# Kernel optimization log

Measured on AMD Instinct MI355X. Metric: run time of the kernel, lower is better.

## Reference

```python
import jax, jax.numpy as jnp
from jax import lax
import numpy as np

T, B, I, H = 512, 64, 512, 512


def setup_inputs() -> dict:
    key = jax.random.key(0)
    k0, k1, k2, k3, k4 = jax.random.split(key, 5)
    s = 1.0 / np.sqrt(H)  # PyTorch LSTM init range
    x = jax.random.normal(k0, (T, B, I), dtype=jnp.float32)
    W_ih = jax.random.uniform(k1, (4 * H, I), jnp.float32, -s, s)
    W_hh = jax.random.uniform(k2, (4 * H, H), jnp.float32, -s, s)
    b_ih = jax.random.uniform(k3, (4 * H,), jnp.float32, -s, s)
    b_hh = jax.random.uniform(k4, (4 * H,), jnp.float32, -s, s)
    return {"x": x, "W_ih": W_ih, "W_hh": W_hh, "b_ih": b_ih, "b_hh": b_hh}


def reference(x, W_ih, W_hh, b_ih, b_hh):
    # x: [T, B, I] (seq-first, like nn.LSTM with batch_first=False)
    Bv = x.shape[1]
    Hv = W_hh.shape[1]
    # Precompute input projections for all timesteps: [T, B, 4H]
    x_proj = jnp.einsum('tbi,gi->tbg', x, W_ih) + b_ih + b_hh

    def step(carry, xp):
        h, c = carry
        gates = xp + h @ W_hh.T  # [B, 4H]
        i, f, g, o = jnp.split(gates, 4, axis=-1)  # PyTorch gate order i,f,g,o
        i = jax.nn.sigmoid(i)
        f = jax.nn.sigmoid(f)
        g = jnp.tanh(g)
        o = jax.nn.sigmoid(o)
        c = f * c + i * g
        h = o * jnp.tanh(c)
        return (h, c), h

    h0 = jnp.zeros((Bv, Hv), dtype=x.dtype)
    c0 = jnp.zeros((Bv, Hv), dtype=x.dtype)
    _, ys = lax.scan(step, (h0, c0), x_proj)
    return ys  # [T, B, H]
```

## Files before the change

### kernel.cpp

```cpp
#include <hip/hip_runtime.h>


#define T_STEPS 512
#define BATCH   64
#define HID     512
#define NB      64

typedef short bf16x8 __attribute__((ext_vector_type(8)));
typedef float f32x4  __attribute__((ext_vector_type(4)));

struct U16B { unsigned long long x, y; };

__device__ __forceinline__ unsigned short f2bf(float f) {
    unsigned int u = __builtin_bit_cast(unsigned int, f);
    u += 0x7FFFu + ((u >> 16) & 1u);
    return (unsigned short)(u >> 16);
}
__device__ __forceinline__ unsigned int pack2(float lo, float hi) {
    return (unsigned int)f2bf(lo) | ((unsigned int)f2bf(hi) << 16);
}
__device__ __forceinline__ uint4 cvt8(const float* __restrict__ p) {
    float4 f0 = *(const float4*)p;
    float4 f1 = *(const float4*)(p + 4);
    uint4 r;
    r.x = pack2(f0.x, f0.y);
    r.y = pack2(f0.z, f0.w);
    r.z = pack2(f1.x, f1.y);
    r.w = pack2(f1.z, f1.w);
    return r;
}
__device__ __forceinline__ void store_cg16(void* p, uint4 v) {
    unsigned long long* q = (unsigned long long*)p;
    U16B u = __builtin_bit_cast(U16B, v);
    __hip_atomic_store(q,     u.x, __ATOMIC_RELAXED, __HIP_MEMORY_SCOPE_AGENT);
    __hip_atomic_store(q + 1, u.y, __ATOMIC_RELAXED, __HIP_MEMORY_SCOPE_AGENT);
}
__device__ __forceinline__ float sigmoidf_(float x) {
    return 1.0f / (1.0f + __expf(-x));
}
__device__ __forceinline__ float tanhf_(float x) {
    x = fminf(fmaxf(x, -15.f), 15.f);
    float e = __expf(2.0f * x);
    return (e - 1.0f) / (e + 1.0f);
}

extern "C" __global__ void __launch_bounds__(256, 1)
lstm_fused(const float* __restrict__ x,
           const float* __restrict__ W_ih,
           const float* __restrict__ W_hh,
           const float* __restrict__ b_ih,
           const float* __restrict__ b_hh,
           float* __restrict__ out,
           unsigned int* __restrict__ hbuf)
{
    __shared__ uint4 sB[2][2][16][64];
    __shared__ __align__(16) unsigned int sHt[4][16][8];
    __shared__ __align__(16) float        sHf[4][16][8];

    const int blk  = blockIdx.x;
    const int tid  = threadIdx.x;
    const int w    = tid >> 6;
    const int lane = tid & 63;
    const int l15  = lane & 15;
    const int quad = lane >> 4;
    const int hc0  = blk * 8;

    for (int u = tid; u < 2 * 16 * 64; u += 256) {
        int nt   = u >> 10;
        int kk   = (u >> 6) & 15;
        int ln   = u & 63;
        int c    = (ln & 15) + (nt << 4);
        int grow = ((c >> 3) << 9) + hc0 + (c & 7);
        int k0   = kk * 32 + ((ln >> 4) << 3);
        sB[0][nt][kk][ln] = cvt8(W_ih + grow * 512 + k0);
        sB[1][nt][kk][ln] = cvt8(W_hh + grow * 512 + k0);
    }

    float bias0, bias1;
    {
        int c0 = l15,      g0 = ((c0 >> 3) << 9) + hc0 + (c0 & 7);
        int c1 = l15 + 16, g1 = ((c1 >> 3) << 9) + hc0 + (c1 & 7);
        bias0 = b_ih[g0] + b_hh[g0];
        bias1 = b_ih[g1] + b_hh[g1];
    }
    __syncthreads();

    float cst[4] = {0.f, 0.f, 0.f, 0.f};
    const int aoff = (((w << 4) + l15) * 512) + (quad << 3);
    char* const hb_base  = (char*)hbuf;
    const int   hread_off = (quad << 11) + (((w << 4) + l15) << 5);
    long long budget = 2000000LL;

    for (int t = 0; t < T_STEPS; ++t) {
        f32x4 acc0 = {0.f, 0.f, 0.f, 0.f};
        f32x4 acc1 = {0.f, 0.f, 0.f, 0.f};

        const float* xt = x + (size_t)t * (BATCH * 512) + aoff;
#pragma unroll
        for (int kk = 0; kk < 16; ++kk) {
            bf16x8 a  = __builtin_bit_cast(bf16x8, cvt8(xt + kk * 32));
            bf16x8 b0 = __builtin_bit_cast(bf16x8, sB[0][0][kk][lane]);
            bf16x8 b1 = __builtin_bit_cast(bf16x8, sB[0][1][kk][lane]);
            acc0 = __builtin_amdgcn_mfma_f32_16x16x32_bf16(a, b0, acc0, 0, 0, 0);
            acc1 = __builtin_amdgcn_mfma_f32_16x16x32_bf16(a, b1, acc1, 0, 0, 0);
        }

        if (t > 0) {
            const char* hp = hb_base + (((t - 1) & 1) << 17) + hread_off;
            const unsigned int tgt = (unsigned int)t;
            unsigned long long hw[64];
            for (;;) {
#pragma unroll
                for (int kk = 0; kk < 16; ++kk) {
                    const unsigned long long* q =
                        (const unsigned long long*)(hp + (kk << 13));
#pragma unroll
                    for (int j = 0; j < 4; ++j)
                        hw[kk * 4 + j] = __hip_atomic_load(q + j, __ATOMIC_RELAXED,
                                                           __HIP_MEMORY_SCOPE_AGENT);
                }
                unsigned int m = 0;
#pragma unroll
                for (int i = 0; i < 64; ++i)
                    m |= ((unsigned int)hw[i] ^ tgt) & 0xffffu;
                if (__all(m == 0)) break;
                if (--budget < 0) break;
            }
#pragma unroll
            for (int kk = 0; kk < 16; ++kk) {
                unsigned int w0 = (unsigned int)(hw[4 * kk + 0]);
                unsigned int w1 = (unsigned int)(hw[4 * kk + 0] >> 32);
                unsigned int w2 = (unsigned int)(hw[4 * kk + 1]);
                unsigned int w3 = (unsigned int)(hw[4 * kk + 1] >> 32);
                unsigned int w4 = (unsigned int)(hw[4 * kk + 2]);
                unsigned int w5 = (unsigned int)(hw[4 * kk + 2] >> 32);
                unsigned int w6 = (unsigned int)(hw[4 * kk + 3]);
                unsigned int w7 = (unsigned int)(hw[4 * kk + 3] >> 32);
                uint4 u;
                u.x = (w0 >> 16) | (w1 & 0xffff0000u);
                u.y = (w2 >> 16) | (w3 & 0xffff0000u);
                u.z = (w4 >> 16) | (w5 & 0xffff0000u);
                u.w = (w6 >> 16) | (w7 & 0xffff0000u);
                bf16x8 a  = __builtin_bit_cast(bf16x8, u);
                bf16x8 b0 = __builtin_bit_cast(bf16x8, sB[1][0][kk][lane]);
                bf16x8 b1 = __builtin_bit_cast(bf16x8, sB[1][1][kk][lane]);
                acc0 = __builtin_amdgcn_mfma_f32_16x16x32_bf16(a, b0, acc0, 0, 0, 0);
                acc1 = __builtin_amdgcn_mfma_f32_16x16x32_bf16(a, b1, acc1, 0, 0, 0);
            }
        }

        float gi[4], gf[4], gg[4], go[4];
#pragma unroll
        for (int r = 0; r < 4; ++r) {
            float a0 = acc0[r] + bias0;
            float a1 = acc1[r] + bias1;
            float p0 = __shfl_xor(a0, 8, 64);
            float p1 = __shfl_xor(a1, 8, 64);
            gi[r] = a0; gg[r] = a1; gf[r] = p0; go[r] = p1;
        }
        const unsigned int tagv = (unsigned int)(t + 1);
        if (l15 < 8) {
#pragma unroll
            for (int r = 0; r < 4; ++r) {
                float iv = sigmoidf_(gi[r]);
                float fv = sigmoidf_(gf[r]);
                float gv = tanhf_(gg[r]);
                float ov = sigmoidf_(go[r]);
                cst[r] = fv * cst[r] + iv * gv;
                float hv = ov * tanhf_(cst[r]);
                sHt[w][(quad << 2) + r][l15] =
                    ((unsigned int)f2bf(hv) << 16) | tagv;
                sHf[w][(quad << 2) + r][l15] = hv;
            }
        }
        asm volatile("s_waitcnt lgkmcnt(0)" ::: "memory");
        if (lane < 32) {
            int row  = lane >> 1;
            int half = lane & 1;
            uint4 v = *(const uint4*)&sHt[w][row][half << 2];
            char* dst = hb_base + ((t & 1) << 17) + (blk << 11)
                        + (((w << 4) + row) << 5) + (half << 4);
            store_cg16(dst, v);
        }

        if (lane < 32) {
            int row  = lane & 15;
            int half = lane >> 4;
            uint4 v = *(const uint4*)&sHf[w][row][half << 2];
            float* op = out + (size_t)t * (BATCH * HID)
                        + (size_t)((w << 4) + row) * HID + hc0 + (half << 2);
            *(uint4*)op = v;
        }
    }
}

extern "C" void kernel_launch(void* const* d_in, const int* in_sizes, int n_in,
                              void* d_out, int out_size, void* d_ws, size_t ws_size,
                              hipStream_t stream) {
    const float* x    = (const float*)d_in[0];
    const float* W_ih = (const float*)d_in[1];
    const float* W_hh = (const float*)d_in[2];
    const float* b_ih = (const float*)d_in[3];
    const float* b_hh = (const float*)d_in[4];
    float* out = (float*)d_out;

    unsigned int* hbuf = (unsigned int*)d_ws;
    (void)hipMemsetAsync(hbuf, 0, 2 * NB * 64 * 8 * sizeof(unsigned int), stream);

    hipLaunchKernelGGL(lstm_fused, dim3(NB), dim3(256), 0, stream,
                       x, W_ih, W_hh, b_ih, b_hh, out, hbuf);
}
```

Measured before the change: 4.037 ms.

## Pin persistent LSTM workgroups to one XCC and widen per-block hidden slice

The kernel launches a large grid and lets only workgroups that land on XCC 0 claim one of 32 ticket slots; the rest exit. All cooperating blocks therefore share one L2 for the h-exchange. Each block now owns 16 hidden units across all four gates, so every lane computes the full gate set without cross-lane shuffles. The h buffer is re-laid out so each row is contiguous, and it is polled with inline-asm dwordx4 loads using sc0. The trade-off is half as many CUs, more MFMA work per block, and reliance on how workgroups are dispatched across XCCs.

```diff
diff --git a/kernel.cpp b/kernel.cpp
--- a/kernel.cpp
+++ b/kernel.cpp
@@ -4,12 +4,13 @@
 #define T_STEPS 512
 #define BATCH   64
 #define HID     512
-#define NB      64
+#define NW      32
+#define GRID    2048
+#define HBUF_BYTES (1 << 18)
 
 typedef short bf16x8 __attribute__((ext_vector_type(8)));
 typedef float f32x4  __attribute__((ext_vector_type(4)));
-
-struct U16B { unsigned long long x, y; };
+typedef unsigned int u32x4 __attribute__((ext_vector_type(4)));
 
 __device__ __forceinline__ unsigned short f2bf(float f) {
     unsigned int u = __builtin_bit_cast(unsigned int, f);
@@ -19,22 +20,16 @@
 __device__ __forceinline__ unsigned int pack2(float lo, float hi) {
     return (unsigned int)f2bf(lo) | ((unsigned int)f2bf(hi) << 16);
 }
-__device__ __forceinline__ uint4 cvt8(const float* __restrict__ p) {
+__device__ __forceinline__ u32x4 cvt8(const float* __restrict__ p) {
     float4 f0 = *(const float4*)p;
     float4 f1 = *(const float4*)(p + 4);
-    uint4 r;
+    u32x4 r;
     r.x = pack2(f0.x, f0.y);
     r.y = pack2(f0.z, f0.w);
     r.z = pack2(f1.x, f1.y);
     r.w = pack2(f1.z, f1.w);
     return r;
 }
-__device__ __forceinline__ void store_cg16(void* p, uint4 v) {
-    unsigned long long* q = (unsigned long long*)p;
-    U16B u = __builtin_bit_cast(U16B, v);
-    __hip_atomic_store(q,     u.x, __ATOMIC_RELAXED, __HIP_MEMORY_SCOPE_AGENT);
-    __hip_atomic_store(q + 1, u.y, __ATOMIC_RELAXED, __HIP_MEMORY_SCOPE_AGENT);
-}
 __device__ __forceinline__ float sigmoidf_(float x) {
     return 1.0f / (1.0f + __expf(-x));
 }
@@ -43,6 +38,23 @@
     float e = __expf(2.0f * x);
     return (e - 1.0f) / (e + 1.0f);
 }
+
+#define VAL4(A) do { \
+    m |= ((A.x ^ tgt) & 0xffffu); m |= ((A.y ^ tgt) & 0xffffu); \
+    m |= ((A.z ^ tgt) & 0xffffu); m |= ((A.w ^ tgt) & 0xffffu); } while (0)
+
+#define FRAGMFMA(KK, A, B) do { \
+    u32x4 u_; \
+    u_.x = (A.x >> 16) | (A.y & 0xffff0000u); \
+    u_.y = (A.z >> 16) | (A.w & 0xffff0000u); \
+    u_.z = (B.x >> 16) | (B.y & 0xffff0000u); \
+    u_.w = (B.z >> 16) | (B.w & 0xffff0000u); \
+    bf16x8 a_ = __builtin_bit_cast(bf16x8, u_); \
+    acc0 = __builtin_amdgcn_mfma_f32_16x16x32_bf16(a_, __builtin_bit_cast(bf16x8, sB[1][0][KK][lane]), acc0, 0, 0, 0); \
+    acc1 = __builtin_amdgcn_mfma_f32_16x16x32_bf16(a_, __builtin_bit_cast(bf16x8, sB[1][1][KK][lane]), acc1, 0, 0, 0); \
+    acc2 = __builtin_amdgcn_mfma_f32_16x16x32_bf16(a_, __builtin_bit_cast(bf16x8, sB[1][2][KK][lane]), acc2, 0, 0, 0); \
+    acc3 = __builtin_amdgcn_mfma_f32_16x16x32_bf16(a_, __builtin_bit_cast(bf16x8, sB[1][3][KK][lane]), acc3, 0, 0, 0); \
+} while (0)
 
 extern "C" __global__ void __launch_bounds__(256, 1)
 lstm_fused(const float* __restrict__ x,
@@ -51,145 +63,176 @@
            const float* __restrict__ b_ih,
            const float* __restrict__ b_hh,
            float* __restrict__ out,
-           unsigned int* __restrict__ hbuf)
+           unsigned int* __restrict__ hbuf,
+           unsigned int* __restrict__ tickets)
 {
-    __shared__ uint4 sB[2][2][16][64];
-    __shared__ __align__(16) unsigned int sHt[4][16][8];
-    __shared__ __align__(16) float        sHf[4][16][8];
-
-    const int blk  = blockIdx.x;
-    const int tid  = threadIdx.x;
+    __shared__ u32x4 sB[2][4][16][64];
+    __shared__ __align__(16) unsigned int sHt[4][16][16];
+    __shared__ __align__(16) float        sHf[4][16][16];
+    __shared__ int sWid;
+
+    const int tid = threadIdx.x;
+
+    if (tid == 0) {
+        unsigned int xcc;
+        asm volatile("s_getreg_b32 %0, hwreg(HW_REG_XCC_ID)" : "=s"(xcc));
+        int id = -1;
+        if ((xcc & 0xfu) == 0u) {
+            unsigned int tk = __hip_atomic_fetch_add(tickets, 1u,
+                                 __ATOMIC_RELAXED, __HIP_MEMORY_SCOPE_AGENT);
+            if (tk < NW) id = (int)tk;
+        }
+        sWid = id;
+    }
+    __syncthreads();
+    const int wid = sWid;
+    if (wid < 0) return;
+
     const int w    = tid >> 6;
     const int lane = tid & 63;
     const int l15  = lane & 15;
     const int quad = lane >> 4;
-    const int hc0  = blk * 8;
-
-    for (int u = tid; u < 2 * 16 * 64; u += 256) {
-        int nt   = u >> 10;
+    const int hc0  = wid << 4;
+
+    for (int u = tid; u < 2 * 4 * 16 * 64; u += 256) {
+        int m    = u >> 12;
+        int nt   = (u >> 10) & 3;
         int kk   = (u >> 6) & 15;
         int ln   = u & 63;
-        int c    = (ln & 15) + (nt << 4);
-        int grow = ((c >> 3) << 9) + hc0 + (c & 7);
-        int k0   = kk * 32 + ((ln >> 4) << 3);
-        sB[0][nt][kk][ln] = cvt8(W_ih + grow * 512 + k0);
-        sB[1][nt][kk][ln] = cvt8(W_hh + grow * 512 + k0);
-    }
-
-    float bias0, bias1;
+        int grow = (nt << 9) + hc0 + (ln & 15);
+        int k0   = (kk << 5) + ((ln >> 4) << 3);
+        sB[m][nt][kk][ln] = cvt8((m ? W_hh : W_ih) + grow * 512 + k0);
+    }
+
+    float bias0, bias1, bias2, bias3;
     {
-        int c0 = l15,      g0 = ((c0 >> 3) << 9) + hc0 + (c0 & 7);
-        int c1 = l15 + 16, g1 = ((c1 >> 3) << 9) + hc0 + (c1 & 7);
-        bias0 = b_ih[g0] + b_hh[g0];
-        bias1 = b_ih[g1] + b_hh[g1];
+        int c = hc0 + l15;
+        bias0 = b_ih[c]        + b_hh[c];
+        bias1 = b_ih[c + 512]  + b_hh[c + 512];
+        bias2 = b_ih[c + 1024] + b_hh[c + 1024];
+        bias3 = b_ih[c + 1536] + b_hh[c + 1536];
     }
     __syncthreads();
 
     float cst[4] = {0.f, 0.f, 0.f, 0.f};
-    const int aoff = (((w << 4) + l15) * 512) + (quad << 3);
-    char* const hb_base  = (char*)hbuf;
-    const int   hread_off = (quad << 11) + (((w << 4) + l15) << 5);
-    long long budget = 2000000LL;
+    const int arow = (w << 4) + l15;
+    const int aoff = arow * 512 + (quad << 3);
+    char* const hb = (char*)hbuf;
+    char* const hrd_base = hb + arow * 2048 + (quad << 5);
+    long long budget = 300000LL;
 
     for (int t = 0; t < T_STEPS; ++t) {
-        f32x4 acc0 = {0.f, 0.f, 0.f, 0.f};
-        f32x4 acc1 = {0.f, 0.f, 0.f, 0.f};
+        f32x4 acc0 = {0.f,0.f,0.f,0.f}, acc1 = {0.f,0.f,0.f,0.f};
+        f32x4 acc2 = {0.f,0.f,0.f,0.f}, acc3 = {0.f,0.f,0.f,0.f};
 
         const float* xt = x + (size_t)t * (BATCH * 512) + aoff;
 #pragma unroll
         for (int kk = 0; kk < 16; ++kk) {
-            bf16x8 a  = __builtin_bit_cast(bf16x8, cvt8(xt + kk * 32));
-            bf16x8 b0 = __builtin_bit_cast(bf16x8, sB[0][0][kk][lane]);
-            bf16x8 b1 = __builtin_bit_cast(bf16x8, sB[0][1][kk][lane]);
-            acc0 = __builtin_amdgcn_mfma_f32_16x16x32_bf16(a, b0, acc0, 0, 0, 0);
-            acc1 = __builtin_amdgcn_mfma_f32_16x16x32_bf16(a, b1, acc1, 0, 0, 0);
+            bf16x8 a = __builtin_bit_cast(bf16x8, cvt8(xt + kk * 32));
+            acc0 = __builtin_amdgcn_mfma_f32_16x16x32_bf16(a, __builtin_bit_cast(bf16x8, sB[0][0][kk][lane]), acc0, 0, 0, 0);
+            acc1 = __builtin_amdgcn_mfma_f32_16x16x32_bf16(a, __builtin_bit_cast(bf16x8, sB[0][1][kk][lane]), acc1, 0, 0, 0);
+            acc2 = __builtin_amdgcn_mfma_f32_16x16x32_bf16(a, __builtin_bit_cast(bf16x8, sB[0][2][kk][lane]), acc2, 0, 0, 0);
+            acc3 = __builtin_amdgcn_mfma_f32_16x16x32_bf16(a, __builtin_bit_cast(bf16x8, sB[0][3][kk][lane]), acc3, 0, 0, 0);
         }
 
         if (t > 0) {
-            const char* hp = hb_base + (((t - 1) & 1) << 17) + hread_off;
+            const char* hrd = hrd_base + (((t - 1) & 1) << 17);
             const unsigned int tgt = (unsigned int)t;
-            unsigned long long hw[64];
+            u32x4 h0,h1,h2,h3,h4,h5,h6,h7,h8,h9,h10,h11,h12,h13,h14,h15,
+                  h16,h17,h18,h19,h20,h21,h22,h23,h24,h25,h26,h27,h28,h29,h30,h31;
             for (;;) {
-#pragma unroll
-                for (int kk = 0; kk < 16; ++kk) {
-                    const unsigned long long* q =
-                        (const unsigned long long*)(hp + (kk << 13));
-#pragma unroll
-                    for (int j = 0; j < 4; ++j)
-                        hw[kk * 4 + j] = __hip_atomic_load(q + j, __ATOMIC_RELAXED,
-                                                           __HIP_MEMORY_SCOPE_AGENT);
-                }
+                asm volatile(
+                    "global_load_dwordx4 %[h0],  %[a], off offset:0 sc0\n\t"
+                    "global_load_dwordx4 %[h1],  %[a], off offset:16 sc0\n\t"
+                    "global_load_dwordx4 %[h2],  %[a], off offset:128 sc0\n\t"
+                    "global_load_dwordx4 %[h3],  %[a], off offset:144 sc0\n\t"
+                    "global_load_dwordx4 %[h4],  %[a], off offset:256 sc0\n\t"
+                    "global_load_dwordx4 %[h5],  %[a], off offset:272 sc0\n\t"
+                    "global_load_dwordx4 %[h6],  %[a], off offset:384 sc0\n\t"
+                    "global_load_dwordx4 %[h7],  %[a], off offset:400 sc0\n\t"
+                    "global_load_dwordx4 %[h8],  %[a], off offset:512 sc0\n\t"
+                    "global_load_dwordx4 %[h9],  %[a], off offset:528 sc0\n\t"
+                    "global_load_dwordx4 %[h10], %[a], off offset:640 sc0\n\t"
+                    "global_load_dwordx4 %[h11], %[a], off offset:656 sc0\n\t"
+                    "global_load_dwordx4 %[h12], %[a], off offset:768 sc0\n\t"
+                    "global_load_dwordx4 %[h13], %[a], off offset:784 sc0\n\t"
+                    "global_load_dwordx4 %[h14], %[a], off offset:896 sc0\n\t"
+                    "global_load_dwordx4 %[h15], %[a], off offset:912 sc0\n\t"
+                    "global_load_dwordx4 %[h16], %[a], off offset:1024 sc0\n\t"
+                    "global_load_dwordx4 %[h17], %[a], off offset:1040 sc0\n\t"
+                    "global_load_dwordx4 %[h18], %[a], off offset:1152 sc0\n\t"
+                    "global_load_dwordx4 %[h19], %[a], off offset:1168 sc0\n\t"
+                    "global_load_dwordx4 %[h20], %[a], off offset:1280 sc0\n\t"
+                    "global_load_dwordx4 %[h21], %[a], off offset:1296 sc0\n\t"
+                    "global_load_dwordx4 %[h22], %[a], off offset:1408 sc0\n\t"
+                    "global_load_dwordx4 %[h23], %[a], off offset:1424 sc0\n\t"
+                    "global_load_dwordx4 %[h24], %[a], off offset:1536 sc0\n\t"
+                    "global_load_dwordx4 %[h25], %[a], off offset:1552 sc0\n\t"
+                    "global_load_dwordx4 %[h26], %[a], off offset:1664 sc0\n\t"
+                    "global_load_dwordx4 %[h27], %[a], off offset:1680 sc0\n\t"
+                    "global_load_dwordx4 %[h28], %[a], off offset:1792 sc0\n\t"
+                    "global_load_dwordx4 %[h29], %[a], off offset:1808 sc0\n\t"
+                    "global_load_dwordx4 %[h30], %[a], off offset:1920 sc0\n\t"
+                    "global_load_dwordx4 %[h31], %[a], off offset:1936 sc0\n\t"
+                    "s_waitcnt vmcnt(0)"
+                    : [h0]"=&v"(h0),  [h1]"=&v"(h1),  [h2]"=&v"(h2),  [h3]"=&v"(h3),
+                      [h4]"=&v"(h4),  [h5]"=&v"(h5),  [h6]"=&v"(h6),  [h7]"=&v"(h7),
+                      [h8]"=&v"(h8),  [h9]"=&v"(h9),  [h10]"=&v"(h10),[h11]"=&v"(h11),
+                      [h12]"=&v"(h12),[h13]"=&v"(h13),[h14]"=&v"(h14),[h15]"=&v"(h15),
+                      [h16]"=&v"(h16),[h17]"=&v"(h17),[h18]"=&v"(h18),[h19]"=&v"(h19),
+                      [h20]"=&v"(h20),[h21]"=&v"(h21),[h22]"=&v"(h22),[h23]"=&v"(h23),
+                      [h24]"=&v"(h24),[h25]"=&v"(h25),[h26]"=&v"(h26),[h27]"=&v"(h27),
+                      [h28]"=&v"(h28),[h29]"=&v"(h29),[h30]"=&v"(h30),[h31]"=&v"(h31)
+                    : [a]"v"(hrd)
+                    : "memory");
                 unsigned int m = 0;
-#pragma unroll
-                for (int i = 0; i < 64; ++i)
-                    m |= ((unsigned int)hw[i] ^ tgt) & 0xffffu;
+                VAL4(h0);  VAL4(h1);  VAL4(h2);  VAL4(h3);
+                VAL4(h4);  VAL4(h5);  VAL4(h6);  VAL4(h7);
+                VAL4(h8);  VAL4(h9);  VAL4(h10); VAL4(h11);
+                VAL4(h12); VAL4(h13); VAL4(h14); VAL4(h15);
+                VAL4(h16); VAL4(h17); VAL4(h18); VAL4(h19);
+                VAL4(h20); VAL4(h21); VAL4(h22); VAL4(h23);
+                VAL4(h24); VAL4(h25); VAL4(h26); VAL4(h27);
+                VAL4(h28); VAL4(h29); VAL4(h30); VAL4(h31);
                 if (__all(m == 0)) break;
                 if (--budget < 0) break;
             }
-#pragma unroll
-            for (int kk = 0; kk < 16; ++kk) {
-                unsigned int w0 = (unsigned int)(hw[4 * kk + 0]);
-                unsigned int w1 = (unsigned int)(hw[4 * kk + 0] >> 32);
-                unsigned int w2 = (unsigned int)(hw[4 * kk + 1]);
-                unsigned int w3 = (unsigned int)(hw[4 * kk + 1] >> 32);
-                unsigned int w4 = (unsigned int)(hw[4 * kk + 2]);
-                unsigned int w5 = (unsigned int)(hw[4 * kk + 2] >> 32);
-                unsigned int w6 = (unsigned int)(hw[4 * kk + 3]);
-                unsigned int w7 = (unsigned int)(hw[4 * kk + 3] >> 32);
-                uint4 u;
-                u.x = (w0 >> 16) | (w1 & 0xffff0000u);
-                u.y = (w2 >> 16) | (w3 & 0xffff0000u);
-                u.z = (w4 >> 16) | (w5 & 0xffff0000u);
-                u.w = (w6 >> 16) | (w7 & 0xffff0000u);
-                bf16x8 a  = __builtin_bit_cast(bf16x8, u);
-                bf16x8 b0 = __builtin_bit_cast(bf16x8, sB[1][0][kk][lane]);
-                bf16x8 b1 = __builtin_bit_cast(bf16x8, sB[1][1][kk][lane]);
-                acc0 = __builtin_amdgcn_mfma_f32_16x16x32_bf16(a, b0, acc0, 0, 0, 0);
-                acc1 = __builtin_amdgcn_mfma_f32_16x16x32_bf16(a, b1, acc1, 0, 0, 0);
-            }
-        }
-
-        float gi[4], gf[4], gg[4], go[4];
+            FRAGMFMA(0,  h0,  h1);  FRAGMFMA(1,  h2,  h3);
+            FRAGMFMA(2,  h4,  h5);  FRAGMFMA(3,  h6,  h7);
+            FRAGMFMA(4,  h8,  h9);  FRAGMFMA(5,  h10, h11);
+            FRAGMFMA(6,  h12, h13); FRAGMFMA(7,  h14, h15);
+            FRAGMFMA(8,  h16, h17); FRAGMFMA(9,  h18, h19);
+            FRAGMFMA(10, h20, h21); FRAGMFMA(11, h22, h23);
+            FRAGMFMA(12, h24, h25); FRAGMFMA(13, h26, h27);
+            FRAGMFMA(14, h28, h29); FRAGMFMA(15, h30, h31);
+        }
+
+        const unsigned int tagv = (unsigned int)(t + 1);
 #pragma unroll
         for (int r = 0; r < 4; ++r) {
-            float a0 = acc0[r] + bias0;
-            float a1 = acc1[r] + bias1;
-            float p0 = __shfl_xor(a0, 8, 64);
-            float p1 = __shfl_xor(a1, 8, 64);
-            gi[r] = a0; gg[r] = a1; gf[r] = p0; go[r] = p1;
-        }
-        const unsigned int tagv = (unsigned int)(t + 1);
-        if (l15 < 8) {
-#pragma unroll
-            for (int r = 0; r < 4; ++r) {
-                float iv = sigmoidf_(gi[r]);
-                float fv = sigmoidf_(gf[r]);
-                float gv = tanhf_(gg[r]);
-                float ov = sigmoidf_(go[r]);
-                cst[r] = fv * cst[r] + iv * gv;
-                float hv = ov * tanhf_(cst[r]);
-                sHt[w][(quad << 2) + r][l15] =
-                    ((unsigned int)f2bf(hv) << 16) | tagv;
-                sHf[w][(quad << 2) + r][l15] = hv;
-            }
+            float iv = sigmoidf_(acc0[r] + bias0);
+            float fv = sigmoidf_(acc1[r] + bias1);
+            float gv = tanhf_(acc2[r] + bias2);
+            float ov = sigmoidf_(acc3[r] + bias3);
+            cst[r] = fv * cst[r] + iv * gv;
+            float hv = ov * tanhf_(cst[r]);
+            sHt[w][(quad << 2) + r][l15] =
+                ((unsigned int)f2bf(hv) << 16) | tagv;
+            sHf[w][(quad << 2) + r][l15] = hv;
         }
         asm volatile("s_waitcnt lgkmcnt(0)" ::: "memory");
-        if (lane < 32) {
-            int row  = lane >> 1;
-            int half = lane & 1;
-            uint4 v = *(const uint4*)&sHt[w][row][half << 2];
-            char* dst = hb_base + ((t & 1) << 17) + (blk << 11)
-                        + (((w << 4) + row) << 5) + (half << 4);
-            store_cg16(dst, v);
-        }
-
-        if (lane < 32) {
-            int row  = lane & 15;
-            int half = lane >> 4;
-            uint4 v = *(const uint4*)&sHf[w][row][half << 2];
+
+        {
+            int row16 = lane >> 2, seg = lane & 3;
+            u32x4 v = *(const u32x4*)&sHt[w][row16][seg << 2];
+            char* dst = hb + ((t & 1) << 17) + (((w << 4) + row16) * 2048)
+                        + (hc0 << 2) + (seg << 4);
+            asm volatile("global_store_dwordx4 %0, %1, off sc0"
+                         :: "v"(dst), "v"(v) : "memory");
+            u32x4 vf = *(const u32x4*)&sHf[w][row16][seg << 2];
             float* op = out + (size_t)t * (BATCH * HID)
-                        + (size_t)((w << 4) + row) * HID + hc0 + (half << 2);
-            *(uint4*)op = v;
+                        + (size_t)((w << 4) + row16) * HID + hc0 + (seg << 2);
+            *(u32x4*)op = vf;
         }
     }
 }
@@ -204,9 +247,10 @@
     const float* b_hh = (const float*)d_in[4];
     float* out = (float*)d_out;
 
-    unsigned int* hbuf = (unsigned int*)d_ws;
-    (void)hipMemsetAsync(hbuf, 0, 2 * NB * 64 * 8 * sizeof(unsigned int), stream);
-
-    hipLaunchKernelGGL(lstm_fused, dim3(NB), dim3(256), 0, stream,
-                       x, W_ih, W_hh, b_ih, b_hh, out, hbuf);
-}
+    unsigned int* hbuf    = (unsigned int*)d_ws;
+    unsigned int* tickets = (unsigned int*)((char*)d_ws + HBUF_BYTES);
+    (void)hipMemsetAsync(d_ws, 0, HBUF_BYTES + 64, stream);
+
+    hipLaunchKernelGGL(lstm_fused, dim3(GRID), dim3(256), 0, stream,
+                       x, W_ih, W_hh, b_ih, b_hh, out, hbuf, tickets);
+}
```

Measured after the change: 5.369 ms. 1.33x slower.

## Precompute next step's input projection after publishing h to hide x loads

Applied to the files above, without the earlier changes.

The x·W_ih MFMA for timestep t+1 now runs after the h state for step t has been published, so the global loads of x and their matmul overlap with other blocks' recurrent work instead of sitting on the critical path at the start of each step. The x loads are issued into registers before the h publish, and sched_barriers stop the compiler from reordering across them. The h publish is also changed from two 8-byte stores by 32 lanes to a single 8-byte atomic store by all 64 lanes. The cost is 128 extra registers for prefetched x, and an extra redundant projection on the last step.

```diff
diff --git a/kernel.cpp b/kernel.cpp
--- a/kernel.cpp
+++ b/kernel.cpp
@@ -9,8 +9,6 @@
 typedef short bf16x8 __attribute__((ext_vector_type(8)));
 typedef float f32x4  __attribute__((ext_vector_type(4)));
 
-struct U16B { unsigned long long x, y; };
-
 __device__ __forceinline__ unsigned short f2bf(float f) {
     unsigned int u = __builtin_bit_cast(unsigned int, f);
     u += 0x7FFFu + ((u >> 16) & 1u);
@@ -19,9 +17,7 @@
 __device__ __forceinline__ unsigned int pack2(float lo, float hi) {
     return (unsigned int)f2bf(lo) | ((unsigned int)f2bf(hi) << 16);
 }
-__device__ __forceinline__ uint4 cvt8(const float* __restrict__ p) {
-    float4 f0 = *(const float4*)p;
-    float4 f1 = *(const float4*)(p + 4);
+__device__ __forceinline__ uint4 pack8(float4 f0, float4 f1) {
     uint4 r;
     r.x = pack2(f0.x, f0.y);
     r.y = pack2(f0.z, f0.w);
@@ -29,11 +25,10 @@
     r.w = pack2(f1.z, f1.w);
     return r;
 }
-__device__ __forceinline__ void store_cg16(void* p, uint4 v) {
-    unsigned long long* q = (unsigned long long*)p;
-    U16B u = __builtin_bit_cast(U16B, v);
-    __hip_atomic_store(q,     u.x, __ATOMIC_RELAXED, __HIP_MEMORY_SCOPE_AGENT);
-    __hip_atomic_store(q + 1, u.y, __ATOMIC_RELAXED, __HIP_MEMORY_SCOPE_AGENT);
+__device__ __forceinline__ uint4 cvt8(const float* __restrict__ p) {
+    float4 f0 = *(const float4*)p;
+    float4 f1 = *(const float4*)(p + 4);
+    return pack8(f0, f1);
 }
 __device__ __forceinline__ float sigmoidf_(float x) {
     return 1.0f / (1.0f + __expf(-x));
@@ -91,19 +86,29 @@
     const int   hread_off = (quad << 11) + (((w << 4) + l15) << 5);
     long long budget = 2000000LL;
 
-    for (int t = 0; t < T_STEPS; ++t) {
-        f32x4 acc0 = {0.f, 0.f, 0.f, 0.f};
-        f32x4 acc1 = {0.f, 0.f, 0.f, 0.f};
-
-        const float* xt = x + (size_t)t * (BATCH * 512) + aoff;
+    float4 xr[32];
+    f32x4 accx0 = {0.f, 0.f, 0.f, 0.f};
+    f32x4 accx1 = {0.f, 0.f, 0.f, 0.f};
+    {
+        const float* x0 = x + aoff;
 #pragma unroll
         for (int kk = 0; kk < 16; ++kk) {
-            bf16x8 a  = __builtin_bit_cast(bf16x8, cvt8(xt + kk * 32));
+            xr[2 * kk]     = *(const float4*)(x0 + kk * 32);
+            xr[2 * kk + 1] = *(const float4*)(x0 + kk * 32 + 4);
+        }
+#pragma unroll
+        for (int kk = 0; kk < 16; ++kk) {
+            bf16x8 a  = __builtin_bit_cast(bf16x8, pack8(xr[2 * kk], xr[2 * kk + 1]));
             bf16x8 b0 = __builtin_bit_cast(bf16x8, sB[0][0][kk][lane]);
             bf16x8 b1 = __builtin_bit_cast(bf16x8, sB[0][1][kk][lane]);
-            acc0 = __builtin_amdgcn_mfma_f32_16x16x32_bf16(a, b0, acc0, 0, 0, 0);
-            acc1 = __builtin_amdgcn_mfma_f32_16x16x32_bf16(a, b1, acc1, 0, 0, 0);
-        }
+            accx0 = __builtin_amdgcn_mfma_f32_16x16x32_bf16(a, b0, accx0, 0, 0, 0);
+            accx1 = __builtin_amdgcn_mfma_f32_16x16x32_bf16(a, b1, accx1, 0, 0, 0);
+        }
+    }
+
+    for (int t = 0; t < T_STEPS; ++t) {
+        f32x4 acc0 = accx0;
+        f32x4 acc1 = accx1;
 
         if (t > 0) {
             const char* hp = hb_base + (((t - 1) & 1) << 17) + hread_off;
@@ -174,15 +179,28 @@
             }
         }
         asm volatile("s_waitcnt lgkmcnt(0)" ::: "memory");
-        if (lane < 32) {
-            int row  = lane >> 1;
-            int half = lane & 1;
-            uint4 v = *(const uint4*)&sHt[w][row][half << 2];
+
+        {
+            const int tn = (t + 1 < T_STEPS) ? (t + 1) : t;
+            const float* xn = x + (size_t)tn * (BATCH * 512) + aoff;
+#pragma unroll
+            for (int kk = 0; kk < 16; ++kk) {
+                xr[2 * kk]     = *(const float4*)(xn + kk * 32);
+                xr[2 * kk + 1] = *(const float4*)(xn + kk * 32 + 4);
+            }
+        }
+        __builtin_amdgcn_sched_barrier(0);
+
+        {
+            int row  = lane >> 2;
+            int pair = lane & 3;
+            unsigned long long v =
+                *(const unsigned long long*)&sHt[w][row][pair << 1];
             char* dst = hb_base + ((t & 1) << 17) + (blk << 11)
-                        + (((w << 4) + row) << 5) + (half << 4);
-            store_cg16(dst, v);
-        }
-
+                        + (((w << 4) + row) << 5) + (pair << 3);
+            __hip_atomic_store((unsigned long long*)dst, v,
+                               __ATOMIC_RELAXED, __HIP_MEMORY_SCOPE_AGENT);
+        }
         if (lane < 32) {
             int row  = lane & 15;
             int half = lane >> 4;
@@ -190,6 +208,18 @@
             float* op = out + (size_t)t * (BATCH * HID)
                         + (size_t)((w << 4) + row) * HID + hc0 + (half << 2);
             *(uint4*)op = v;
+        }
+        __builtin_amdgcn_sched_barrier(0);
+
+        accx0 = (f32x4){0.f, 0.f, 0.f, 0.f};
+        accx1 = (f32x4){0.f, 0.f, 0.f, 0.f};
+#pragma unroll
+        for (int kk = 0; kk < 16; ++kk) {
+            bf16x8 a  = __builtin_bit_cast(bf16x8, pack8(xr[2 * kk], xr[2 * kk + 1]));
+            bf16x8 b0 = __builtin_bit_cast(bf16x8, sB[0][0][kk][lane]);
+            bf16x8 b1 = __builtin_bit_cast(bf16x8, sB[0][1][kk][lane]);
+            accx0 = __builtin_amdgcn_mfma_f32_16x16x32_bf16(a, b0, accx0, 0, 0, 0);
+            accx1 = __builtin_amdgcn_mfma_f32_16x16x32_bf16(a, b1, accx1, 0, 0, 0);
         }
     }
 }
```

Result: slower. 4.836 ms (+19.8%).
